# Kernel optimization log

Measured on AMD Instinct MI355X. Metric: run time of the kernel, lower is better.

Reference implementation:

```python
import jax, jax.numpy as jnp
import numpy as np
from jax import lax

# Static module configuration (mirrors init_kwargs)
L = 64
KH, KW = 4, 7          # kernel_size (h, w), h = w // 2 + 1
DH, DW = 1, 1          # kernel_dilation
EXCLUSIVE = True
RECEP_H = (KH - 1) * DH + 1
RECEP_W = (KW - 1) * DW + 1
BATCH, IN_F, OUT_F = 4096, 64, 64


def _autoregressive_mask():
    # netket MaskedConv2D mask: full rows above the last; last row only sees
    # columns strictly left of center (exclusive=True).
    m = np.ones((KH, KW, 1, 1), np.float32)
    m[-1, KW // 2 + (0 if EXCLUSIVE else 1):, :, :] = 0.0
    return jnp.asarray(m)


def setup_inputs() -> dict:
    key = jax.random.key(0)
    k1, k2, k3, k4 = jax.random.split(key, 4)
    inputs = jax.random.normal(k1, (BATCH, IN_F), jnp.float32)
    cache = jax.random.normal(k2, (BATCH, RECEP_H, L, IN_F), jnp.float32)
    kernel = jax.random.normal(k3, (KH, KW, IN_F, OUT_F), jnp.float32) * 0.05
    bias = jax.random.normal(k4, (OUT_F,), jnp.float32) * 0.05
    return {"inputs": inputs, "cache": cache, "kernel": kernel,
            "bias": bias, "index": 1000}


def reference(inputs, cache, kernel, bias, index):
    batch, in_f = inputs.shape
    kernel = kernel * _autoregressive_mask()  # masked kernel, as at init

    index_w = index % L
    index_w_in = (index - int(EXCLUSIVE)) % L
    inp4 = inputs[:, None, None, :]  # (B, 1, 1, F)

    def _add(c):
        # -1 row start: jax wraps negative starts -> write into last cache row
        return lax.dynamic_update_slice(c, inp4, (0, -1, index_w_in, 0))

    def _shift(c):
        # shift rows up, zero-fill new last row
        return jnp.pad(c[:, 1:, :, :], ((0, 0), (0, 1), (0, 0), (0, 0)))

    cache_new_row = jnp.where(index_w_in == 0, _add(_shift(cache)), _shift(_add(cache)))
    cache_new = jnp.where(index_w == 0, cache_new_row, _add(cache))
    cache = jnp.where(index - int(EXCLUSIVE) >= 0, cache_new, cache)

    # pad width for 'SAME'-style receptive field, then slice the window at index_w
    padded = jnp.pad(cache, ((0, 0), (0, 0),
                             (KW // 2 * DW, (KW - 1) // 2 * DW), (0, 0)))
    window = lax.dynamic_slice(padded, (0, 0, index_w, 0),
                               (batch, RECEP_H, RECEP_W, in_f))  # (B, rh, rw, F)

    y = lax.conv_general_dilated(window, kernel, window_strides=(1, 1),
                                 padding='VALID', rhs_dilation=(DH, DW),
                                 dimension_numbers=('NHWC', 'HWIO', 'NHWC'))
    y = y + bias  # (B, 1, 1, OUT_F)
    return y[:, 0, 0, :], cache
```

## Files before the change

### kernel.cpp

```cpp
#include <hip/hip_runtime.h>

#define NB_CONV 256
#define NB_COPY 1536
#define NTHR 256

__global__ __launch_bounds__(256)
void fmc_fused(const float* __restrict__ inputs,
               const float* __restrict__ cache,
               const float* __restrict__ wk,
               const float* __restrict__ bias,
               const int* __restrict__ idxp,
               float* __restrict__ y_out,
               float* __restrict__ cache_out)
{
    const int idx = idxp[0];
    int iw = idx % 64;        if (iw < 0)  iw += 64;
    int iwi = (idx - 1) % 64; if (iwi < 0) iwi += 64;
    const bool upd = (idx - 1) >= 0;
    const int tid = threadIdx.x;

    if (blockIdx.x < NB_CONV) {
        __shared__ float Ws[64][68];
        __shared__ float Xs[64][18];
        const int bbase = blockIdx.x * 16;
        const int fog = tid & 15;
        const int bp  = tid >> 4;

        float acc[2][4];
        if (tid < 128) {
            const float4 bv = *(const float4*)(bias + (fog << 2));
            acc[0][0]=bv.x; acc[0][1]=bv.y; acc[0][2]=bv.z; acc[0][3]=bv.w;
            acc[1][0]=bv.x; acc[1][1]=bv.y; acc[1][2]=bv.z; acc[1][3]=bv.w;
        }

        for (int kh = 0; kh < 4; ++kh) {
            for (int kw = 0; kw < 7; ++kw) {
                if (kh == 3 && kw >= 3) break;
                const int col = iw - 3 + kw;
                int kind;
                int hs = kh;
                if (col < 0 || col >= 64) kind = 0;
                else if (!upd) kind = 2;
                else if (iw != 0) kind = (kh == 3 && col == iwi) ? 1 : 2;
                else if (iwi != 0) {
                    if (kh == 3) kind = 0;
                    else if (kh == 2 && col == iwi) kind = 1;
                    else { kind = 2; hs = kh + 1; }
                } else {
                    if (kh == 3) kind = (col == 0) ? 1 : 0;
                    else { kind = 2; hs = kh + 1; }
                }

                __syncthreads();
                const float* wt = wk + (kh * 7 + kw) * 4096;
                #pragma unroll
                for (int i = 0; i < 4; ++i) {
                    const int f4 = tid + (i << 8);
                    const int ci = f4 >> 4;
                    const int fo = (f4 & 15) << 2;
                    const float4 v = *(const float4*)(wt + ci * 64 + fo);
                    *(float4*)&Ws[ci][fo] = v;
                }
                {
                    const int bl = tid >> 4;
                    const int c4 = (tid & 15) << 2;
                    float4 v = make_float4(0.f, 0.f, 0.f, 0.f);
                    if (kind == 1)
                        v = *(const float4*)(inputs + (bbase + bl) * 64 + c4);
                    else if (kind == 2)
                        v = *(const float4*)(cache + ((((bbase + bl) << 2) + hs) * 64 + col) * 64 + c4);
                    Xs[c4 + 0][bl] = v.x;
                    Xs[c4 + 1][bl] = v.y;
                    Xs[c4 + 2][bl] = v.z;
                    Xs[c4 + 3][bl] = v.w;
                }
                __syncthreads();

                if (tid < 128) {
                    #pragma unroll 16
                    for (int ci = 0; ci < 64; ++ci) {
                        const float4 w = *(const float4*)&Ws[ci][fog << 2];
                        const float2 x = *(const float2*)&Xs[ci][bp << 1];
                        acc[0][0] = fmaf(x.x, w.x, acc[0][0]);
                        acc[0][1] = fmaf(x.x, w.y, acc[0][1]);
                        acc[0][2] = fmaf(x.x, w.z, acc[0][2]);
                        acc[0][3] = fmaf(x.x, w.w, acc[0][3]);
                        acc[1][0] = fmaf(x.y, w.x, acc[1][0]);
                        acc[1][1] = fmaf(x.y, w.y, acc[1][1]);
                        acc[1][2] = fmaf(x.y, w.z, acc[1][2]);
                        acc[1][3] = fmaf(x.y, w.w, acc[1][3]);
                    }
                }
            }
        }
        if (tid < 128) {
            float* y0 = y_out + (bbase + (bp << 1)) * 64 + (fog << 2);
            *(float4*)y0        = make_float4(acc[0][0], acc[0][1], acc[0][2], acc[0][3]);
            *(float4*)(y0 + 64) = make_float4(acc[1][0], acc[1][1], acc[1][2], acc[1][3]);
        }
    } else {
        const float4* __restrict__ c4 = (const float4*)cache;
        const float4* __restrict__ i4 = (const float4*)inputs;
        float4* __restrict__ o4 = (float4*)cache_out;
        const int t0 = (blockIdx.x - NB_CONV) * NTHR + tid;
        const int stride = NB_COPY * NTHR;
        const int total = 4096 * 4096;
        if (!upd) {
            for (int i = t0; i < total; i += stride) o4[i] = c4[i];
        } else if (iw != 0) {
            const int target = 3 * 1024 + iwi * 16;
            for (int i = t0; i < total; i += stride) {
                const int r = i & 4095;
                const float4* src = c4 + i;
                if ((r & ~15) == target)
                    src = i4 + ((i >> 12) << 4) + (r & 15);
                o4[i] = *src;
            }
        } else if (iwi != 0) {
            for (int i = t0; i < total; i += stride) {
                const int r = i & 4095;
                const int h = r >> 10;
                float4 v = make_float4(0.f, 0.f, 0.f, 0.f);
                if (h == 2 && ((r >> 4) & 63) == iwi) v = i4[((i >> 12) << 4) + (r & 15)];
                else if (h < 3) v = c4[i + 1024];
                o4[i] = v;
            }
        } else {
            for (int i = t0; i < total; i += stride) {
                const int r = i & 4095;
                const int h = r >> 10;
                float4 v = make_float4(0.f, 0.f, 0.f, 0.f);
                if (h == 3) { if (((r >> 4) & 63) == 0) v = i4[((i >> 12) << 4) + (r & 15)]; }
                else v = c4[i + 1024];
                o4[i] = v;
            }
        }
    }
}

extern "C" void kernel_launch(void* const* d_in, const int* in_sizes, int n_in,
                              void* d_out, int out_size, void* d_ws, size_t ws_size,
                              hipStream_t stream) {
    const float* inputs = (const float*)d_in[0];
    const float* cache  = (const float*)d_in[1];
    const float* wk     = (const float*)d_in[2];
    const float* bias   = (const float*)d_in[3];
    const int*   idxp   = (const int*)d_in[4];
    float* y_out = (float*)d_out;
    float* cache_out = (float*)d_out + 4096 * 64;
    fmc_fused<<<NB_CONV + NB_COPY, NTHR, 0, stream>>>(inputs, cache, wk, bias, idxp,
                                                      y_out, cache_out);
}
```

Before: 110.5 us.

## Use nontemporal unrolled copy and size grid from occupancy query

The cache-copy path now uses nontemporal loads and stores, with the common index path unrolled four-way so more loads are in flight. The grid size is computed from a runtime occupancy query (256 CUs times resident blocks) instead of a fixed copy block count. Launch bounds request 8 blocks per CU and the shared-memory padding on Ws/Xs is removed, which may add LDS bank conflicts in the conv part. The occupancy query runs on every launch and adds host overhead.

```diff
diff --git a/kernel.cpp b/kernel.cpp
--- a/kernel.cpp
+++ b/kernel.cpp
@@ -1,17 +1,19 @@
 #include <hip/hip_runtime.h>
 
 #define NB_CONV 256
-#define NB_COPY 1536
 #define NTHR 256
 
-__global__ __launch_bounds__(256)
+typedef float f4 __attribute__((ext_vector_type(4)));
+
+__global__ __launch_bounds__(256, 8)
 void fmc_fused(const float* __restrict__ inputs,
                const float* __restrict__ cache,
                const float* __restrict__ wk,
                const float* __restrict__ bias,
                const int* __restrict__ idxp,
                float* __restrict__ y_out,
-               float* __restrict__ cache_out)
+               float* __restrict__ cache_out,
+               int nb_copy)
 {
     const int idx = idxp[0];
     int iw = idx % 64;        if (iw < 0)  iw += 64;
@@ -20,15 +22,15 @@
     const int tid = threadIdx.x;
 
     if (blockIdx.x < NB_CONV) {
-        __shared__ float Ws[64][68];
-        __shared__ float Xs[64][18];
+        __shared__ float Ws[64][64];
+        __shared__ float Xs[64][16];
         const int bbase = blockIdx.x * 16;
         const int fog = tid & 15;
         const int bp  = tid >> 4;
 
         float acc[2][4];
         if (tid < 128) {
-            const float4 bv = *(const float4*)(bias + (fog << 2));
+            const f4 bv = *(const f4*)(bias + (fog << 2));
             acc[0][0]=bv.x; acc[0][1]=bv.y; acc[0][2]=bv.z; acc[0][3]=bv.w;
             acc[1][0]=bv.x; acc[1][1]=bv.y; acc[1][2]=bv.z; acc[1][3]=bv.w;
         }
@@ -55,20 +57,19 @@
                 const float* wt = wk + (kh * 7 + kw) * 4096;
                 #pragma unroll
                 for (int i = 0; i < 4; ++i) {
-                    const int f4 = tid + (i << 8);
-                    const int ci = f4 >> 4;
-                    const int fo = (f4 & 15) << 2;
-                    const float4 v = *(const float4*)(wt + ci * 64 + fo);
-                    *(float4*)&Ws[ci][fo] = v;
+                    const int f4i = tid + (i << 8);
+                    const int ci = f4i >> 4;
+                    const int fo = (f4i & 15) << 2;
+                    *(f4*)&Ws[ci][fo] = *(const f4*)(wt + ci * 64 + fo);
                 }
                 {
                     const int bl = tid >> 4;
                     const int c4 = (tid & 15) << 2;
-                    float4 v = make_float4(0.f, 0.f, 0.f, 0.f);
+                    f4 v = (f4)(0.f);
                     if (kind == 1)
-                        v = *(const float4*)(inputs + (bbase + bl) * 64 + c4);
+                        v = *(const f4*)(inputs + (bbase + bl) * 64 + c4);
                     else if (kind == 2)
-                        v = *(const float4*)(cache + ((((bbase + bl) << 2) + hs) * 64 + col) * 64 + c4);
+                        v = *(const f4*)(cache + ((((bbase + bl) << 2) + hs) * 64 + col) * 64 + c4);
                     Xs[c4 + 0][bl] = v.x;
                     Xs[c4 + 1][bl] = v.y;
                     Xs[c4 + 2][bl] = v.z;
@@ -77,9 +78,9 @@
                 __syncthreads();
 
                 if (tid < 128) {
-                    #pragma unroll 16
+                    #pragma unroll 8
                     for (int ci = 0; ci < 64; ++ci) {
-                        const float4 w = *(const float4*)&Ws[ci][fog << 2];
+                        const f4 w = *(const f4*)&Ws[ci][fog << 2];
                         const float2 x = *(const float2*)&Xs[ci][bp << 1];
                         acc[0][0] = fmaf(x.x, w.x, acc[0][0]);
                         acc[0][1] = fmaf(x.x, w.y, acc[0][1]);
@@ -95,44 +96,71 @@
         }
         if (tid < 128) {
             float* y0 = y_out + (bbase + (bp << 1)) * 64 + (fog << 2);
-            *(float4*)y0        = make_float4(acc[0][0], acc[0][1], acc[0][2], acc[0][3]);
-            *(float4*)(y0 + 64) = make_float4(acc[1][0], acc[1][1], acc[1][2], acc[1][3]);
+            *(f4*)y0        = (f4){acc[0][0], acc[0][1], acc[0][2], acc[0][3]};
+            *(f4*)(y0 + 64) = (f4){acc[1][0], acc[1][1], acc[1][2], acc[1][3]};
         }
     } else {
-        const float4* __restrict__ c4 = (const float4*)cache;
-        const float4* __restrict__ i4 = (const float4*)inputs;
-        float4* __restrict__ o4 = (float4*)cache_out;
+        const f4* __restrict__ c4 = (const f4*)cache;
+        const f4* __restrict__ i4 = (const f4*)inputs;
+        f4* __restrict__ o4 = (f4*)cache_out;
         const int t0 = (blockIdx.x - NB_CONV) * NTHR + tid;
-        const int stride = NB_COPY * NTHR;
+        const int stride = nb_copy * NTHR;
         const int total = 4096 * 4096;
         if (!upd) {
-            for (int i = t0; i < total; i += stride) o4[i] = c4[i];
+            int i = t0;
+            for (; i + 3 * stride < total; i += 4 * stride) {
+                f4 v[4];
+                #pragma unroll
+                for (int u = 0; u < 4; ++u)
+                    v[u] = __builtin_nontemporal_load(c4 + i + u * stride);
+                #pragma unroll
+                for (int u = 0; u < 4; ++u)
+                    __builtin_nontemporal_store(v[u], o4 + i + u * stride);
+            }
+            for (; i < total; i += stride)
+                __builtin_nontemporal_store(__builtin_nontemporal_load(c4 + i), o4 + i);
         } else if (iw != 0) {
             const int target = 3 * 1024 + iwi * 16;
-            for (int i = t0; i < total; i += stride) {
+            int i = t0;
+            for (; i + 3 * stride < total; i += 4 * stride) {
+                f4 v[4];
+                #pragma unroll
+                for (int u = 0; u < 4; ++u) {
+                    const int j = i + u * stride;
+                    const int r = j & 4095;
+                    const f4* p = ((r & ~15) == target)
+                                  ? (i4 + ((j >> 12) << 4) + (r & 15))
+                                  : (c4 + j);
+                    v[u] = __builtin_nontemporal_load(p);
+                }
+                #pragma unroll
+                for (int u = 0; u < 4; ++u)
+                    __builtin_nontemporal_store(v[u], o4 + i + u * stride);
+            }
+            for (; i < total; i += stride) {
                 const int r = i & 4095;
-                const float4* src = c4 + i;
-                if ((r & ~15) == target)
-                    src = i4 + ((i >> 12) << 4) + (r & 15);
-                o4[i] = *src;
+                const f4* p = ((r & ~15) == target)
+                              ? (i4 + ((i >> 12) << 4) + (r & 15))
+                              : (c4 + i);
+                __builtin_nontemporal_store(__builtin_nontemporal_load(p), o4 + i);
             }
         } else if (iwi != 0) {
             for (int i = t0; i < total; i += stride) {
                 const int r = i & 4095;
                 const int h = r >> 10;
-                float4 v = make_float4(0.f, 0.f, 0.f, 0.f);
+                f4 v = (f4)(0.f);
                 if (h == 2 && ((r >> 4) & 63) == iwi) v = i4[((i >> 12) << 4) + (r & 15)];
                 else if (h < 3) v = c4[i + 1024];
-                o4[i] = v;
+                __builtin_nontemporal_store(v, o4 + i);
             }
         } else {
             for (int i = t0; i < total; i += stride) {
                 const int r = i & 4095;
                 const int h = r >> 10;
-                float4 v = make_float4(0.f, 0.f, 0.f, 0.f);
+                f4 v = (f4)(0.f);
                 if (h == 3) { if (((r >> 4) & 63) == 0) v = i4[((i >> 12) << 4) + (r & 15)]; }
                 else v = c4[i + 1024];
-                o4[i] = v;
+                __builtin_nontemporal_store(v, o4 + i);
             }
         }
     }
@@ -148,6 +176,14 @@
     const int*   idxp   = (const int*)d_in[4];
     float* y_out = (float*)d_out;
     float* cache_out = (float*)d_out + 4096 * 64;
-    fmc_fused<<<NB_CONV + NB_COPY, NTHR, 0, stream>>>(inputs, cache, wk, bias, idxp,
-                                                      y_out, cache_out);
+
+    int occ = 0;
+    if (hipOccupancyMaxActiveBlocksPerMultiprocessor(&occ,
+            reinterpret_cast<const void*>(fmc_fused), NTHR, 0) != hipSuccess || occ < 2)
+        occ = 7;
+    const int nb_total = 256 * occ;
+    const int nb_copy  = nb_total - NB_CONV;
+
+    fmc_fused<<<nb_total, NTHR, 0, stream>>>(inputs, cache, wk, bias, idxp,
+                                             y_out, cache_out, nb_copy);
 }
```

Result: slower. 140.1 us (+26.7%).
